# Optimization experiments

Hardware: AMD Instinct MI355X
Metric: run time of the kernel (lower is better)

The kernel has to match this reference:

```python
import jax, jax.numpy as jnp
import numpy as np

N = 50000      # nodes
D = 128        # input_dim == hidden_dim (required by aggrmethod='add')
E_ADJ = 800000 # nonzeros in sparse adjacency
E_PRED = 500000
L = 2          # nbaselayer
BN_EPS = 1e-5


def setup_inputs() -> dict:
    key = jax.random.key(0)
    ks = jax.random.split(key, 10)
    x = jax.random.normal(ks[0], (N, D), dtype=jnp.float32)
    adj_row = jax.random.randint(ks[1], (E_ADJ,), 0, N, dtype=jnp.int32)
    adj_col = jax.random.randint(ks[2], (E_ADJ,), 0, N, dtype=jnp.int32)
    # positive values ~ normalized adjacency weights (avg degree 16)
    adj_val = jax.random.uniform(ks[3], (E_ADJ,), dtype=jnp.float32) / 16.0
    edge_index = jax.random.randint(ks[4], (2, E_PRED), 0, N, dtype=jnp.int32)
    s = 1.0 / np.sqrt(D).astype(np.float32)
    W = jax.random.uniform(ks[5], (L, D, D), jnp.float32, -s, s)
    W_self = jax.random.uniform(ks[6], (L, D, D), jnp.float32, -s, s)
    b = jax.random.uniform(ks[7], (L, D), jnp.float32, -s, s)
    gamma = jnp.ones((L, D), jnp.float32)
    beta = jnp.zeros((L, D), jnp.float32)
    sc = 1.0 / np.sqrt(2 * D).astype(np.float32)
    Wc = jax.random.uniform(ks[8], (2 * D, 1), jnp.float32, -sc, sc)
    bc = jax.random.uniform(ks[9], (1,), jnp.float32, -sc, sc)
    return dict(x=x, adj_row=adj_row, adj_col=adj_col, adj_val=adj_val,
                edge_index=edge_index, W=W, W_self=W_self, b=b,
                gamma=gamma, beta=beta, Wc=Wc, bc=bc)


def _batchnorm(h, g, be):
    # BatchNorm1d over node dim, training-mode (batch) statistics, biased var
    mu = jnp.mean(h, axis=0)
    var = jnp.mean(jnp.square(h - mu), axis=0)
    return g * (h - mu) * jax.lax.rsqrt(var + BN_EPS) + be


def reference(x, adj_row, adj_col, adj_val, edge_index, W, W_self, b, gamma, beta, Wc, bc):
    h = x
    for i in range(L):  # GraphConvolutionBS layers
        support = h @ W[i]                                  # [N, D]
        # spmm(adj, support): gather by col, scale by val, scatter-add by row
        agg = jax.ops.segment_sum(adj_val[:, None] * support[adj_col],
                                  adj_row, num_segments=N)   # [N, D]
        out = agg + h @ W_self[i] + b[i]                    # self-loop + bias
        h = jax.nn.relu(_batchnorm(out, gamma[i], beta[i]))
        # dropout omitted (eval mode)
    node_emb = h + x  # aggrmethod='add', dense=False: residual with block input
    emb1 = node_emb[edge_index[0]]                          # [E_PRED, D]
    emb2 = node_emb[edge_index[1]]
    edge_emb = jnp.concatenate([emb1, emb2], axis=1)        # [E_PRED, 2D]
    return jax.nn.sigmoid(edge_emb @ Wc + bc)               # [E_PRED, 1]
```

## Files before the change

kernel.cpp:

```cpp
#include <hip/hip_runtime.h>
#include <hip/hip_bf16.h>
#include <hip/hip_fp16.h>

#define DD 128
#define BN_EPS 1e-5f
#define SPMM_BLOCKS 2048
#define SCAT_BLOCKS 2048
#define NSLOT 64
#define CAP 32
#define OVF_MAX 8192

typedef __attribute__((ext_vector_type(8))) short bf16x8;
typedef __attribute__((ext_vector_type(4))) float f32x4;

static __device__ __forceinline__ unsigned short f2bf(float f) {
    __hip_bfloat16 h = __float2bfloat16(f);
    return *reinterpret_cast<unsigned short*>(&h);
}
static __device__ __forceinline__ float bf2f(unsigned short u) {
    return __uint_as_float(((unsigned)u) << 16);
}
static __device__ __forceinline__ unsigned pack_rec(int col, float val) {
    __half h = __float2half(val);
    unsigned hb = *reinterpret_cast<unsigned short*>(&h);
    return (unsigned)col | (hb << 16);
}
static __device__ __forceinline__ float rec_val(unsigned rec) {
    unsigned short hb = (unsigned short)(rec >> 16);
    __half h = *reinterpret_cast<__half*>(&hb);
    return __half2float(h);
}

__global__ __launch_bounds__(256) void prep_zero_k(
    const float* __restrict__ W, const float* __restrict__ Wself,
    unsigned short* __restrict__ Wt4, int* __restrict__ zp, int nz)
{
    if (blockIdx.x < 32) {
        int mat   = blockIdx.x >> 3;
        int chunk = blockIdx.x & 7;
        int layer = mat >> 1;
        const float* src = (mat & 1) ? (Wself + layer * 16384) : (W + layer * 16384);
        unsigned short* dst = Wt4 + (size_t)mat * 16384;
        int base = chunk * 2048 + threadIdx.x * 4;
        #pragma unroll
        for (int rep = 0; rep < 2; rep++) {
            int i = base + rep * 1024;
            float4 v = *(const float4*)&src[i];
            int k = i >> 7, n = i & 127;
            dst[(n + 0) * 128 + k] = f2bf(v.x);
            dst[(n + 1) * 128 + k] = f2bf(v.y);
            dst[(n + 2) * 128 + k] = f2bf(v.z);
            dst[(n + 3) * 128 + k] = f2bf(v.w);
        }
    } else {
        int i = (blockIdx.x - 32) * 256 + threadIdx.x;
        if (i < nz) zp[i] = 0;
    }
}

static __device__ __forceinline__ void scatter_body(
    int j, int nsl, int p,
    const int* __restrict__ arow, const int* __restrict__ acol,
    const float* __restrict__ aval, int* __restrict__ cnt,
    unsigned* __restrict__ bucket, int* __restrict__ ovfc,
    int2* __restrict__ ovf, int E, int rpp)
{
    const int slice = j >> 3;
    const int e0 = (int)((long long)E * slice / nsl);
    const int e1 = (int)((long long)E * (slice + 1) / nsl);
    for (int e = e0 + threadIdx.x; e < e1; e += 256) {
        int r = arow[e];
        if (r / rpp == p) {
            int pos = atomicAdd(&cnt[r], 1);
            unsigned rec = pack_rec(acol[e], aval[e]);
            if (pos < CAP) {
                bucket[(size_t)r * CAP + pos] = rec;
            } else {
                int oi = atomicAdd(ovfc, 1);
                if (oi < OVF_MAX) ovf[oi] = make_int2(r, (int)rec);
            }
        }
    }
}

__global__ __launch_bounds__(256) void gemm_l0_scatter(
    const float* __restrict__ A,
    const unsigned short* __restrict__ Wt, const unsigned short* __restrict__ Wst,
    const float* __restrict__ bias,
    unsigned short* __restrict__ support, float* __restrict__ outb, int N, int gemm_grid,
    const int* __restrict__ arow, const int* __restrict__ acol,
    const float* __restrict__ aval, int* __restrict__ cnt,
    unsigned* __restrict__ bucket, int* __restrict__ ovfc,
    int2* __restrict__ ovf, int E, int rpp)
{
    if (blockIdx.x >= gemm_grid) {
        int j = blockIdx.x - gemm_grid;
        int nsl = (gridDim.x - gemm_grid) >> 3;
        int p = blockIdx.x & 7;
        scatter_body(j, nsl, p, arow, acol, aval, cnt, bucket, ovfc, ovf, E, rpp);
        return;
    }

    const int wave = threadIdx.x >> 6;
    const int lane = threadIdx.x & 63;
    const int m    = lane & 15;
    const int quad = lane >> 4;
    const int row0 = blockIdx.x * 64 + wave * 16;

    int ar = row0 + m; if (ar > N - 1) ar = N - 1;
    const float* Ar = A + (size_t)ar * 128;
    bf16x8 af[4];
    #pragma unroll
    for (int ch = 0; ch < 4; ch++) {
        int k0 = ch * 32 + quad * 8;
        float4 u = *(const float4*)&Ar[k0];
        float4 v = *(const float4*)&Ar[k0 + 4];
        float vals[8] = {u.x, u.y, u.z, u.w, v.x, v.y, v.z, v.w};
        #pragma unroll
        for (int jj = 0; jj < 8; jj++) af[ch][jj] = (short)f2bf(vals[jj]);
    }

    f32x4 acc1[8], acc2[8];
    #pragma unroll
    for (int nt = 0; nt < 8; nt++) { acc1[nt] = (f32x4)(0.f); acc2[nt] = (f32x4)(0.f); }

    #pragma unroll
    for (int nt = 0; nt < 8; nt++) {
        const bf16x8* B1 = (const bf16x8*)(Wt  + ((size_t)(nt * 16 + m)) * 128 + quad * 8);
        const bf16x8* B2 = (const bf16x8*)(Wst + ((size_t)(nt * 16 + m)) * 128 + quad * 8);
        acc1[nt] = __builtin_amdgcn_mfma_f32_16x16x32_bf16(af[0], B1[0],  acc1[nt], 0, 0, 0);
        acc2[nt] = __builtin_amdgcn_mfma_f32_16x16x32_bf16(af[0], B2[0],  acc2[nt], 0, 0, 0);
        acc1[nt] = __builtin_amdgcn_mfma_f32_16x16x32_bf16(af[1], B1[4],  acc1[nt], 0, 0, 0);
        acc2[nt] = __builtin_amdgcn_mfma_f32_16x16x32_bf16(af[1], B2[4],  acc2[nt], 0, 0, 0);
        acc1[nt] = __builtin_amdgcn_mfma_f32_16x16x32_bf16(af[2], B1[8],  acc1[nt], 0, 0, 0);
        acc2[nt] = __builtin_amdgcn_mfma_f32_16x16x32_bf16(af[2], B2[8],  acc2[nt], 0, 0, 0);
        acc1[nt] = __builtin_amdgcn_mfma_f32_16x16x32_bf16(af[3], B1[12], acc1[nt], 0, 0, 0);
        acc2[nt] = __builtin_amdgcn_mfma_f32_16x16x32_bf16(af[3], B2[12], acc2[nt], 0, 0, 0);
    }

    float bv[8];
    #pragma unroll
    for (int nt = 0; nt < 8; nt++) bv[nt] = bias[nt * 16 + m];

    #pragma unroll
    for (int r = 0; r < 4; r++) {
        int orow = row0 + quad * 4 + r;
        if (orow < N) {
            size_t base = (size_t)orow * 128 + m;
            #pragma unroll
            for (int nt = 0; nt < 8; nt++) {
                support[base + nt * 16] = f2bf(acc1[nt][r]);
                outb[base + nt * 16]    = acc2[nt][r] + bv[nt];
            }
        }
    }
}

__global__ __launch_bounds__(256) void gemm_bn_k(
    const float* __restrict__ A,
    const unsigned short* __restrict__ Wt, const unsigned short* __restrict__ Wst,
    const float* __restrict__ bias,
    const float* __restrict__ partials, const float* __restrict__ gamma,
    const float* __restrict__ beta, float invN,
    unsigned short* __restrict__ support, float* __restrict__ outb, int N)
{
    __shared__ float tot[256];
    __shared__ float ssc[128], ssh[128];
    {
        float a = 0.f;
        #pragma unroll 8
        for (int s = 0; s < NSLOT; s++)
            a += partials[(size_t)s * 256 + threadIdx.x];
        tot[threadIdx.x] = a;
    }
    __syncthreads();
    if (threadIdx.x < 128) {
        int c = threadIdx.x;
        float mean = tot[c] * invN;
        float var  = tot[128 + c] * invN - mean * mean;
        float sc   = gamma[c] * rsqrtf(var + BN_EPS);
        ssc[c] = sc;
        ssh[c] = beta[c] - mean * sc;
    }
    __syncthreads();

    const int wave = threadIdx.x >> 6;
    const int lane = threadIdx.x & 63;
    const int m    = lane & 15;
    const int quad = lane >> 4;
    const int row0 = blockIdx.x * 64 + wave * 16;

    int ar = row0 + m; if (ar > N - 1) ar = N - 1;
    const float* Ar = A + (size_t)ar * 128;
    bf16x8 af[4];
    #pragma unroll
    for (int ch = 0; ch < 4; ch++) {
        int k0 = ch * 32 + quad * 8;
        float4 u = *(const float4*)&Ar[k0];
        float4 v = *(const float4*)&Ar[k0 + 4];
        float vals[8] = {u.x, u.y, u.z, u.w, v.x, v.y, v.z, v.w};
        #pragma unroll
        for (int j = 0; j < 8; j++) {
            float val = vals[j] * ssc[k0 + j] + ssh[k0 + j];
            val = val > 0.f ? val : 0.f;
            af[ch][j] = (short)f2bf(val);
        }
    }

    f32x4 acc1[8], acc2[8];
    #pragma unroll
    for (int nt = 0; nt < 8; nt++) { acc1[nt] = (f32x4)(0.f); acc2[nt] = (f32x4)(0.f); }

    #pragma unroll
    for (int nt = 0; nt < 8; nt++) {
        const bf16x8* B1 = (const bf16x8*)(Wt  + ((size_t)(nt * 16 + m)) * 128 + quad * 8);
        const bf16x8* B2 = (const bf16x8*)(Wst + ((size_t)(nt * 16 + m)) * 128 + quad * 8);
        acc1[nt] = __builtin_amdgcn_mfma_f32_16x16x32_bf16(af[0], B1[0],  acc1[nt], 0, 0, 0);
        acc2[nt] = __builtin_amdgcn_mfma_f32_16x16x32_bf16(af[0], B2[0],  acc2[nt], 0, 0, 0);
        acc1[nt] = __builtin_amdgcn_mfma_f32_16x16x32_bf16(af[1], B1[4],  acc1[nt], 0, 0, 0);
        acc2[nt] = __builtin_amdgcn_mfma_f32_16x16x32_bf16(af[1], B2[4],  acc2[nt], 0, 0, 0);
        acc1[nt] = __builtin_amdgcn_mfma_f32_16x16x32_bf16(af[2], B1[8],  acc1[nt], 0, 0, 0);
        acc2[nt] = __builtin_amdgcn_mfma_f32_16x16x32_bf16(af[2], B2[8],  acc2[nt], 0, 0, 0);
        acc1[nt] = __builtin_amdgcn_mfma_f32_16x16x32_bf16(af[3], B1[12], acc1[nt], 0, 0, 0);
        acc2[nt] = __builtin_amdgcn_mfma_f32_16x16x32_bf16(af[3], B2[12], acc2[nt], 0, 0, 0);
    }

    float bv[8];
    #pragma unroll
    for (int nt = 0; nt < 8; nt++) bv[nt] = bias[nt * 16 + m];

    #pragma unroll
    for (int r = 0; r < 4; r++) {
        int orow = row0 + quad * 4 + r;
        if (orow < N) {
            size_t base = (size_t)orow * 128 + m;
            #pragma unroll
            for (int nt = 0; nt < 8; nt++) {
                support[base + nt * 16] = f2bf(acc1[nt][r]);
                outb[base + nt * 16]    = acc2[nt][r] + bv[nt];
            }
        }
    }
}

__global__ __launch_bounds__(256) void spmm_stats_k(
    const int* __restrict__ cnt, const unsigned* __restrict__ bucket,
    const int* __restrict__ ovfc, const int2* __restrict__ ovf,
    const unsigned short* __restrict__ sup, float* __restrict__ outb,
    float* __restrict__ partials, int ngroups, int N)
{
    const int r    = threadIdx.x & 31;
    const int slot = threadIdx.x >> 5;
    float s4[4] = {0.f, 0.f, 0.f, 0.f};
    float q4[4] = {0.f, 0.f, 0.f, 0.f};
    __shared__ float red[8][128];

    for (int g = blockIdx.x; g < ngroups; g += gridDim.x) {
        int row = g * 8 + slot;
        if (row >= N) continue;
        int nrec = cnt[row]; if (nrec > CAP) nrec = CAP;
        const unsigned* packed = bucket + (size_t)row * CAP;

        float4 acc = make_float4(0.f, 0.f, 0.f, 0.f);
        int e = 0;
        for (; e + 4 <= nrec; e += 4) {
            unsigned p0 = packed[e + 0];
            unsigned p1 = packed[e + 1];
            unsigned p2 = packed[e + 2];
            unsigned p3 = packed[e + 3];
            ushort4 s0 = *(const ushort4*)&sup[((size_t)(p0 & 0xFFFFu) << 7) + r * 4];
            ushort4 s1 = *(const ushort4*)&sup[((size_t)(p1 & 0xFFFFu) << 7) + r * 4];
            ushort4 s2 = *(const ushort4*)&sup[((size_t)(p2 & 0xFFFFu) << 7) + r * 4];
            ushort4 s3 = *(const ushort4*)&sup[((size_t)(p3 & 0xFFFFu) << 7) + r * 4];
            float v0 = rec_val(p0), v1 = rec_val(p1);
            float v2 = rec_val(p2), v3 = rec_val(p3);
            acc.x += v0 * bf2f(s0.x); acc.y += v0 * bf2f(s0.y);
            acc.z += v0 * bf2f(s0.z); acc.w += v0 * bf2f(s0.w);
            acc.x += v1 * bf2f(s1.x); acc.y += v1 * bf2f(s1.y);
            acc.z += v1 * bf2f(s1.z); acc.w += v1 * bf2f(s1.w);
            acc.x += v2 * bf2f(s2.x); acc.y += v2 * bf2f(s2.y);
            acc.z += v2 * bf2f(s2.z); acc.w += v2 * bf2f(s2.w);
            acc.x += v3 * bf2f(s3.x); acc.y += v3 * bf2f(s3.y);
            acc.z += v3 * bf2f(s3.z); acc.w += v3 * bf2f(s3.w);
        }
        for (; e < nrec; e++) {
            unsigned pr = packed[e];
            ushort4 sv = *(const ushort4*)&sup[((size_t)(pr & 0xFFFFu) << 7) + r * 4];
            float v = rec_val(pr);
            acc.x += v * bf2f(sv.x); acc.y += v * bf2f(sv.y);
            acc.z += v * bf2f(sv.z); acc.w += v * bf2f(sv.w);
        }

        int oc = *ovfc;
        if (oc > 0) {
            if (oc > OVF_MAX) oc = OVF_MAX;
            for (int i = 0; i < oc; i++) {
                int2 orec = ovf[i];
                if (orec.x == row) {
                    unsigned pr = (unsigned)orec.y;
                    ushort4 sv = *(const ushort4*)&sup[((size_t)(pr & 0xFFFFu) << 7) + r * 4];
                    float v = rec_val(pr);
                    acc.x += v * bf2f(sv.x); acc.y += v * bf2f(sv.y);
                    acc.z += v * bf2f(sv.z); acc.w += v * bf2f(sv.w);
                }
            }
        }

        float4* op = (float4*)&outb[((size_t)row << 7) + r * 4];
        float4 o = *op;
        o.x += acc.x; o.y += acc.y; o.z += acc.z; o.w += acc.w;
        *op = o;
        s4[0] += o.x; s4[1] += o.y; s4[2] += o.z; s4[3] += o.w;
        q4[0] += o.x * o.x; q4[1] += o.y * o.y; q4[2] += o.z * o.z; q4[3] += o.w * o.w;
    }

    #pragma unroll
    for (int j = 0; j < 4; j++) red[slot][r * 4 + j] = s4[j];
    __syncthreads();
    float ts = 0.f;
    if (threadIdx.x < 128) {
        #pragma unroll
        for (int j = 0; j < 8; j++) ts += red[j][threadIdx.x];
    }
    __syncthreads();
    #pragma unroll
    for (int j = 0; j < 4; j++) red[slot][r * 4 + j] = q4[j];
    __syncthreads();
    if (threadIdx.x < 128) {
        float tq = 0.f;
        #pragma unroll
        for (int j = 0; j < 8; j++) tq += red[j][threadIdx.x];
        float* slotp = partials + (size_t)(blockIdx.x & (NSLOT - 1)) * 256;
        atomicAdd(&slotp[threadIdx.x], ts);
        atomicAdd(&slotp[128 + threadIdx.x], tq);
    }
}

__global__ __launch_bounds__(256) void score_k(
    const float* __restrict__ outb, const float* __restrict__ partials,
    const float* __restrict__ gamma, const float* __restrict__ beta,
    const float* __restrict__ x, const float* __restrict__ Wc,
    float* __restrict__ s1, float* __restrict__ s2, float invN, int N)
{
    __shared__ float tot[256];
    __shared__ float sa[128], sb[128];
    {
        float a = 0.f;
        #pragma unroll 8
        for (int s = 0; s < NSLOT; s++)
            a += partials[(size_t)s * 256 + threadIdx.x];
        tot[threadIdx.x] = a;
    }
    __syncthreads();
    if (threadIdx.x < 128) {
        int c = threadIdx.x;
        float mean = tot[c] * invN;
        float var  = tot[128 + c] * invN - mean * mean;
        float sc   = gamma[c] * rsqrtf(var + BN_EPS);
        sa[c] = sc;
        sb[c] = beta[c] - mean * sc;
    }
    __syncthreads();

    int total = N * 32;
    int stride = gridDim.x * 256;
    for (int idx = blockIdx.x * 256 + threadIdx.x; idx < total; idx += stride) {
        int c4 = (idx & 31) * 4;
        float4 o = *(const float4*)&outb[(size_t)idx * 4];
        float res[4];
        const float* op = &o.x;
        #pragma unroll
        for (int j = 0; j < 4; j++) {
            float v = op[j] * sa[c4 + j] + sb[c4 + j];
            res[j] = v > 0.f ? v : 0.f;
        }
        float4 xv = *(const float4*)&x[(size_t)idx * 4];
        res[0] += xv.x; res[1] += xv.y; res[2] += xv.z; res[3] += xv.w;
        float4 w1 = *(const float4*)&Wc[c4];
        float4 w2 = *(const float4*)&Wc[128 + c4];
        float a1 = res[0] * w1.x + res[1] * w1.y + res[2] * w1.z + res[3] * w1.w;
        float a2 = res[0] * w2.x + res[1] * w2.y + res[2] * w2.z + res[3] * w2.w;
        #pragma unroll
        for (int off = 1; off < 32; off <<= 1) {
            a1 += __shfl_xor(a1, off);
            a2 += __shfl_xor(a2, off);
        }
        if ((idx & 31) == 0) {
            int row = idx >> 5;
            s1[row] = a1;
            s2[row] = a2;
        }
    }
}

__global__ __launch_bounds__(256) void edge_pred_k(
    const float* __restrict__ s1, const float* __restrict__ s2,
    const int* __restrict__ ei, const float* __restrict__ bc,
    float* __restrict__ outp, int Ep)
{
    int e = blockIdx.x * 256 + threadIdx.x;
    if (e >= Ep) return;
    float v = s1[ei[e]] + s2[ei[Ep + e]] + bc[0];
    outp[e] = 1.f / (1.f + expf(-v));
}

extern "C" void kernel_launch(void* const* d_in, const int* in_sizes, int n_in,
                              void* d_out, int out_size, void* d_ws, size_t ws_size,
                              hipStream_t stream) {
    const float* x        = (const float*)d_in[0];
    const int*   adj_row  = (const int*)  d_in[1];
    const int*   adj_col  = (const int*)  d_in[2];
    const float* adj_val  = (const float*)d_in[3];
    const int*   ei       = (const int*)  d_in[4];
    const float* W        = (const float*)d_in[5];
    const float* W_self   = (const float*)d_in[6];
    const float* b        = (const float*)d_in[7];
    const float* gamma    = (const float*)d_in[8];
    const float* beta     = (const float*)d_in[9];
    const float* Wc       = (const float*)d_in[10];
    const float* bc       = (const float*)d_in[11];
    float* outp = (float*)d_out;

    int N  = in_sizes[0] / DD;
    int E  = in_sizes[1];
    int Ep = in_sizes[4] / 2;
    float invN = 1.f / (float)N;

    size_t nd = (size_t)N * DD;
    char* p = (char*)d_ws;
    unsigned short* support16 = (unsigned short*)p; p += nd * 2;
    float*          outbA     = (float*)p;          p += nd * 4;
    float*          outbB     = (float*)p;          p += nd * 4;
    unsigned short* Wt4       = (unsigned short*)p; p += 4 * 16384 * 2;
    float*          partialsA = (float*)p;          p += (size_t)NSLOT * 256 * 4;
    float*          partialsB = (float*)p;          p += (size_t)NSLOT * 256 * 4;
    int*            cnt       = (int*)p;            p += (size_t)N * 4;
    int*            ovfc      = (int*)p;            p += 4;
    unsigned*       bucket    = (unsigned*)p;       p += (size_t)N * CAP * 4;
    int2*           ovf       = (int2*)p;           p += (size_t)OVF_MAX * 8;
    float*          s1        = (float*)p;          p += (size_t)N * 4;
    float*          s2        = (float*)p;

    int gemm_tiles = (N + 63) / 64;
    int ngroups    = (N + 7) / 8;
    int rpp        = (N + 7) / 8;
    int nz         = NSLOT * 256 * 2 + N + 1;

    prep_zero_k<<<32 + (nz + 255) / 256, 256, 0, stream>>>(
        W, W_self, Wt4, (int*)partialsA, nz);

    gemm_l0_scatter<<<gemm_tiles + SCAT_BLOCKS, 256, 0, stream>>>(
        x, Wt4, Wt4 + 16384, b, support16, outbA, N, gemm_tiles,
        adj_row, adj_col, adj_val, cnt, bucket, ovfc, ovf, E, rpp);
    spmm_stats_k<<<SPMM_BLOCKS, 256, 0, stream>>>(
        cnt, bucket, ovfc, ovf, support16, outbA, partialsA, ngroups, N);

    gemm_bn_k<<<gemm_tiles, 256, 0, stream>>>(
        outbA, Wt4 + 2 * 16384, Wt4 + 3 * 16384, b + DD,
        partialsA, gamma, beta, invN, support16, outbB, N);
    spmm_stats_k<<<SPMM_BLOCKS, 256, 0, stream>>>(
        cnt, bucket, ovfc, ovf, support16, outbB, partialsB, ngroups, N);

    score_k<<<2048, 256, 0, stream>>>(
        outbB, partialsB, gamma + DD, beta + DD, x, Wc, s1, s2, invN, N);
    edge_pred_k<<<(Ep + 255) / 256, 256, 0, stream>>>(s1, s2, ei, bc, outp, Ep);
}
```

Baseline: 282.9 us.

## Use XCC-aware dynamic work queue for adjacency scatter partitions

```diff
diff --git a/kernel.cpp b/kernel.cpp
--- a/kernel.cpp
+++ b/kernel.cpp
@@ -6,6 +6,7 @@
 #define BN_EPS 1e-5f
 #define SPMM_BLOCKS 2048
 #define SCAT_BLOCKS 2048
+#define NSLICE 256
 #define NSLOT 64
 #define CAP 32
 #define OVF_MAX 8192
@@ -29,6 +30,11 @@
     unsigned short hb = (unsigned short)(rec >> 16);
     __half h = *reinterpret_cast<__half*>(&hb);
     return __half2float(h);
+}
+static __device__ __forceinline__ int xcc_id() {
+    int x;
+    asm volatile("s_getreg_b32 %0, hwreg(HW_REG_XCC_ID)" : "=s"(x));
+    return x & 7;
 }
 
 __global__ __launch_bounds__(256) void prep_zero_k(
@@ -58,16 +64,15 @@
     }
 }
 
-static __device__ __forceinline__ void scatter_body(
-    int j, int nsl, int p,
+static __device__ __forceinline__ void scatter_slice(
+    int slice, int p,
     const int* __restrict__ arow, const int* __restrict__ acol,
     const float* __restrict__ aval, int* __restrict__ cnt,
     unsigned* __restrict__ bucket, int* __restrict__ ovfc,
     int2* __restrict__ ovf, int E, int rpp)
 {
-    const int slice = j >> 3;
-    const int e0 = (int)((long long)E * slice / nsl);
-    const int e1 = (int)((long long)E * (slice + 1) / nsl);
+    const int e0 = (int)((long long)E * slice / NSLICE);
+    const int e1 = (int)((long long)E * (slice + 1) / NSLICE);
     for (int e = e0 + threadIdx.x; e < e1; e += 256) {
         int r = arow[e];
         if (r / rpp == p) {
@@ -91,13 +96,22 @@
     const int* __restrict__ arow, const int* __restrict__ acol,
     const float* __restrict__ aval, int* __restrict__ cnt,
     unsigned* __restrict__ bucket, int* __restrict__ ovfc,
-    int2* __restrict__ ovf, int E, int rpp)
+    int2* __restrict__ ovf, int* __restrict__ wq, int E, int rpp)
 {
     if (blockIdx.x >= gemm_grid) {
-        int j = blockIdx.x - gemm_grid;
-        int nsl = (gridDim.x - gemm_grid) >> 3;
-        int p = blockIdx.x & 7;
-        scatter_body(j, nsl, p, arow, acol, aval, cnt, bucket, ovfc, ovf, E, rpp);
+        __shared__ int sh_slice;
+        int myp = xcc_id();
+        for (int k = 0; k < 8; k++) {
+            int p = (myp + k) & 7;
+            while (true) {
+                if (threadIdx.x == 0) sh_slice = atomicAdd(&wq[p], 1);
+                __syncthreads();
+                int s = sh_slice;
+                __syncthreads();
+                if (s >= NSLICE) break;
+                scatter_slice(s, p, arow, acol, aval, cnt, bucket, ovfc, ovf, E, rpp);
+            }
+        }
         return;
     }
 
@@ -436,6 +450,7 @@
     float*          partialsB = (float*)p;          p += (size_t)NSLOT * 256 * 4;
     int*            cnt       = (int*)p;            p += (size_t)N * 4;
     int*            ovfc      = (int*)p;            p += 4;
+    int*            wq        = (int*)p;            p += 8 * 4;
     unsigned*       bucket    = (unsigned*)p;       p += (size_t)N * CAP * 4;
     int2*           ovf       = (int2*)p;           p += (size_t)OVF_MAX * 8;
     float*          s1        = (float*)p;          p += (size_t)N * 4;
@@ -444,14 +459,14 @@
     int gemm_tiles = (N + 63) / 64;
     int ngroups    = (N + 7) / 8;
     int rpp        = (N + 7) / 8;
-    int nz         = NSLOT * 256 * 2 + N + 1;
+    int nz         = NSLOT * 256 * 2 + N + 1 + 8;
 
     prep_zero_k<<<32 + (nz + 255) / 256, 256, 0, stream>>>(
         W, W_self, Wt4, (int*)partialsA, nz);
 
     gemm_l0_scatter<<<gemm_tiles + SCAT_BLOCKS, 256, 0, stream>>>(
         x, Wt4, Wt4 + 16384, b, support16, outbA, N, gemm_tiles,
-        adj_row, adj_col, adj_val, cnt, bucket, ovfc, ovf, E, rpp);
+        adj_row, adj_col, adj_val, cnt, bucket, ovfc, ovf, wq, E, rpp);
     spmm_stats_k<<<SPMM_BLOCKS, 256, 0, stream>>>(
         cnt, bucket, ovfc, ovf, support16, outbA, partialsA, ngroups, N);
 
```

Result: slower. 470.0 us (+66.2%).
